# Performance work log

Measured on AMD Instinct MI355X. Metric: run time of the kernel, lower is better.

The kernel has to match this reference:

```python
import jax, jax.numpy as jnp
import numpy as np


def _lstm(x, h0, c0, Wih, Whh, b):
    """Single-layer LSTM, batch_first input x: [B,T,D]. PyTorch gate order i,f,g,o.
    Returns (h_seq [T,B,H], h_T [B,H], c_T [B,H])."""
    xs = jnp.swapaxes(x, 0, 1)  # [T,B,D]

    def step(carry, xt):
        h, c = carry
        gates = xt @ Wih.T + h @ Whh.T + b  # [B,4H]
        i, f, g, o = jnp.split(gates, 4, axis=-1)
        c = jax.nn.sigmoid(f) * c + jax.nn.sigmoid(i) * jnp.tanh(g)
        h = jax.nn.sigmoid(o) * jnp.tanh(c)
        return (h, c), h

    (h, c), hs = jax.lax.scan(step, (h0, c0), xs)
    return hs, h, c


def setup_inputs() -> dict:
    key = jax.random.key(0)
    ks = jax.random.split(key, 16)
    B, T, Tf, Tu = 256, 365, 15, 76
    Dh, Df, Du, H = 64, 32, 16, 256
    s = 1.0 / np.sqrt(H)  # torch-style uniform scale, approximated with scaled normals
    return {
        "x_d": jax.random.normal(ks[0], (B, T, Dh), jnp.float32),
        "x_f": jax.random.normal(ks[1], (B, Tf, Df), jnp.float32),
        "x_ff": jax.random.normal(ks[2], (B, Tu, Du), jnp.float32),
        "enc_Wih": jax.random.normal(ks[3], (4 * H, Dh), jnp.float32) * s,
        "enc_Whh": jax.random.normal(ks[4], (4 * H, H), jnp.float32) * s,
        "enc_b": jax.random.normal(ks[5], (4 * H,), jnp.float32) * s,
        "decf_Wih": jax.random.normal(ks[6], (4 * H, Df), jnp.float32) * s,
        "decf_Whh": jax.random.normal(ks[7], (4 * H, H), jnp.float32) * s,
        "decf_b": jax.random.normal(ks[8], (4 * H,), jnp.float32) * s,
        "decu_Wih": jax.random.normal(ks[9], (4 * H, Du), jnp.float32) * s,
        "decu_Whh": jax.random.normal(ks[10], (4 * H, H), jnp.float32) * s,
        "decu_b": jax.random.normal(ks[11], (4 * H,), jnp.float32) * s,
        "head_W": jax.random.normal(ks[12], (1, H), jnp.float32) * s,
        "head_b": jax.random.normal(ks[13], (1,), jnp.float32) * s,
    }


def reference(x_d, x_f, x_ff, enc_Wih, enc_Whh, enc_b,
              decf_Wih, decf_Whh, decf_b, decu_Wih, decu_Whh, decu_b,
              head_W, head_b):
    B = x_d.shape[0]
    H = enc_Whh.shape[1]
    Tf = x_f.shape[1]
    Tu = x_ff.shape[1]
    horizon = Tf + Tu
    h0 = jnp.zeros((B, H), x_d.dtype)
    c0 = jnp.zeros((B, H), x_d.dtype)

    # Encoder over historical sequence
    _, h, c = _lstm(x_d, h0, c0, enc_Wih, enc_Whh, enc_b)

    # Forecast decoder: one LSTM step per horizon step + linear head (dropout = eval identity)
    hs_f, h, c = _lstm(x_f, h, c, decf_Wih, decf_Whh, decf_b)  # [Tf,B,H]
    out_f = (jnp.einsum('tbh,oh->tbo', hs_f, head_W)[..., 0] + head_b[0]).T  # [B,Tf]

    # Future decoder, continuing the hidden state
    hs_u, h, c = _lstm(x_ff, h, c, decu_Wih, decu_Whh, decu_b)  # [Tu,B,H]
    out_u = (jnp.einsum('tbh,oh->tbo', hs_u, head_W)[..., 0] + head_b[0]).T  # [B,Tu]

    # Faithful to original: both loops write outputs[:, t], so the future loop
    # overwrites the first Tu columns.
    outputs = jnp.zeros((B, horizon), x_d.dtype)
    outputs = outputs.at[:, :Tf].set(out_f)
    outputs = outputs.at[:, :Tu].set(out_u)
    return outputs
```

## Files before the change

### kernel.cpp

```cpp
#include <hip/hip_runtime.h>
#include <stdint.h>


typedef __attribute__((ext_vector_type(8))) short short8;
typedef __attribute__((ext_vector_type(4))) float f32x4;
typedef __attribute__((ext_vector_type(2))) unsigned int u32x2;
typedef __attribute__((ext_vector_type(4))) unsigned int u32x4;

#define L2E 1.4426950408889634f

__device__ __forceinline__ uint16_t f2bf(float f) {
  uint32_t x = __float_as_uint(f);
  x += 0x7fffu + ((x >> 16) & 1u);
  return (uint16_t)(x >> 16);
}
__device__ __forceinline__ uint32_t cvtpk(float lo, float hi) {
  uint32_t r;
  asm("v_cvt_pk_bf16_f32 %0, %1, %2" : "=v"(r) : "v"(lo), "v"(hi));
  return r;
}
__device__ __forceinline__ float bfhalf(uint32_t w, int hi) {
  return __uint_as_float(hi ? (w & 0xffff0000u) : (w << 16));
}
__device__ __forceinline__ f32x4 MFMA(short8 a, short8 b, f32x4 c) {
  return __builtin_amdgcn_mfma_f32_16x16x32_bf16(a, b, c, 0, 0, 0);
}
__device__ __forceinline__ float ex2(float x) { return __builtin_amdgcn_exp2f(x); }
__device__ __forceinline__ float rcp(float x) { return __builtin_amdgcn_rcpf(x); }

__device__ __forceinline__ short8 pack8s(const float* s, float sc) {
  float4 q0 = *(const float4*)s, q1 = *(const float4*)(s + 4);
  u32x4 t;
  t[0] = cvtpk(q0.x * sc, q0.y * sc);
  t[1] = cvtpk(q0.z * sc, q0.w * sc);
  t[2] = cvtpk(q1.x * sc, q1.y * sc);
  t[3] = cvtpk(q1.z * sc, q1.w * sc);
  return *(short8*)&t;
}

__device__ __forceinline__ void lgkm_barrier() {
  __builtin_amdgcn_sched_barrier(0);
  asm volatile("s_waitcnt lgkmcnt(0)" ::: "memory");
  __builtin_amdgcn_s_barrier();
  __builtin_amdgcn_sched_barrier(0);
}
__device__ __forceinline__ void vm_drain4() {
  __builtin_amdgcn_sched_barrier(0);
  asm volatile("s_waitcnt vmcnt(4)" ::: "memory");
  __builtin_amdgcn_sched_barrier(0);
}

__global__ void init_kernel(float* c_state, uint16_t* h_state, float* out) {
  int i = blockIdx.x * 256 + threadIdx.x;
  if (i < 65536) { c_state[i] = 0.f; h_state[i] = 0; }
  if (i < 256 * 91) out[i] = 0.f;
}

template <int DIN>
__device__ __forceinline__ void xproj_body(
    const float* __restrict__ x, const float* __restrict__ Wih,
    const float* __restrict__ bias, uint32_t* __restrict__ xp,
    int T, int blk, int tid) {
  const int w = tid >> 6, l = tid & 63;
  const int l16 = l & 15, lg = l >> 4;
  const int tc = blk >> 1;
  const int sub = blk & 1;
  const int t = tc;
  constexpr int KT = (DIN + 31) / 32;

  short8 bfr[8][KT];
  float4 bias4[8];
#pragma unroll
  for (int ni = 0; ni < 8; ++ni) {
    const int n = (w * 8 + ni) * 16 + l16;
    bias4[ni] = *(const float4*)&bias[(w * 8 + ni) * 16 + lg * 4];
#pragma unroll
    for (int kt = 0; kt < KT; ++kt) {
      const int k0 = kt * 32 + lg * 8;
      short8 fr;
#pragma unroll
      for (int e = 0; e < 8; ++e) fr[e] = 0;
      if (k0 + 8 <= DIN) fr = pack8s(Wih + (size_t)n * DIN + k0, 1.f);
      bfr[ni][kt] = fr;
    }
  }

  for (int mi = 0; mi < 8; ++mi) {
    const int btile = sub * 8 + mi;
    const int b = btile * 16 + l16;
    short8 af[KT];
#pragma unroll
    for (int kt = 0; kt < KT; ++kt) {
      const int k0 = kt * 32 + lg * 8;
      short8 fr;
#pragma unroll
      for (int e = 0; e < 8; ++e) fr[e] = 0;
      if (k0 + 8 <= DIN) fr = pack8s(x + ((size_t)b * T + t) * DIN + k0, 1.f);
      af[kt] = fr;
    }
#pragma unroll
    for (int ni = 0; ni < 8; ++ni) {
      f32x4 acc = {0.f, 0.f, 0.f, 0.f};
#pragma unroll
      for (int kt = 0; kt < KT; ++kt) acc = MFMA(bfr[ni][kt], af[kt], acc);
      const int nt = w * 8 + ni;
      const float sc = ((nt >> 4) == 2) ? (2.f * L2E) : -L2E;
      size_t idx = ((((size_t)tc * 16 + btile) * 64 + nt) * 64 + l) * 2;
      u32x2 v;
      v[0] = cvtpk((acc[0] + bias4[ni].x) * sc, (acc[1] + bias4[ni].y) * sc);
      v[1] = cvtpk((acc[2] + bias4[ni].z) * sc, (acc[3] + bias4[ni].w) * sc);
      *(u32x2*)(xp + idx) = v;
    }
  }
}

template <int DIN>
__global__ __launch_bounds__(512) void xproj_kernel(
    const float* __restrict__ x, const float* __restrict__ Wih,
    const float* __restrict__ bias, uint32_t* __restrict__ xp,
    int t0, int T) {
  const int tid = threadIdx.x;
  const int blk = blockIdx.x + t0 * 2;
  xproj_body<DIN>(x, Wih, bias, xp - (size_t)t0 * 131072, T, blk, tid);
}

__global__ __launch_bounds__(512) void xproj_mega(
    const float* __restrict__ x0, const float* __restrict__ Wih0,
    const float* __restrict__ b0, uint32_t* __restrict__ xp0,
    const float* __restrict__ x1, const float* __restrict__ Wih1,
    const float* __restrict__ b1, uint32_t* __restrict__ xp1,
    const float* __restrict__ x2, const float* __restrict__ Wih2,
    const float* __restrict__ b2, uint32_t* __restrict__ xp2,
    float* __restrict__ out, uint32_t* __restrict__ flags,
    int T0, int T1, int T2) {
  const int tid = threadIdx.x;
  const int n0 = T0 * 2, n1 = T1 * 2, n2 = T2 * 2;
  const int b = blockIdx.x;
  if (b < n0) {
    xproj_body<64>(x0, Wih0, b0, xp0, T0, b, tid);
  } else if (b < n0 + n1) {
    xproj_body<32>(x1, Wih1, b1, xp1, T1, b - n0, tid);
  } else if (b < n0 + n1 + n2) {
    xproj_body<16>(x2, Wih2, b2, xp2, T2, b - n0 - n1, tid);
  } else {
    for (int i = tid; i < 256 * 15; i += 512)
      out[(size_t)(i / 15) * 91 + 76 + (i % 15)] = 0.f;
    if (tid < 96) flags[tid] = 0;
  }
}

template <int DO_HEAD, int ZINIT>
__global__ __launch_bounds__(512, 2) void rec_kernel(
    const uint32_t* __restrict__ xp, const float* __restrict__ Whh,
    float* __restrict__ c_state, uint16_t* __restrict__ h_state,
    float* __restrict__ out, const float* __restrict__ headW,
    const float* __restrict__ headb, int ct, int tcol0) {
  __shared__ short8 B_lds[8 * 16 * 64];
  __shared__ uint16_t h_lds[2][16][264];
  __shared__ float headbuf[2][16][8];

  const int tid = threadIdx.x, w = tid >> 6, l = tid & 63;
  const int l16 = l & 15, lg = l >> 4;
  const int blk = blockIdx.x, b0 = blk * 16;

  short8 bv[48];
#pragma unroll
  for (int g = 0; g < 4; ++g) {
    const float wsc = (g == 2) ? (2.f * L2E) : -L2E;
#pragma unroll
    for (int nt = 0; nt < 2; ++nt)
#pragma unroll
      for (int kt = 0; kt < 8; ++kt) {
        const int row = (g * 16 + w * 2 + nt) * 16 + l16;
        const float* s = Whh + (size_t)row * 256 + kt * 32 + lg * 8;
        short8 fr;
#pragma unroll
        for (int e = 0; e < 8; ++e) fr[e] = (short)f2bf(s[e] * wsc);
        const int tile = g * 2 + nt;
        if (kt <= 5) bv[tile * 6 + kt] = fr;
        else B_lds[(w * 16 + (kt - 6) * 8 + tile) * 64 + l] = fr;
      }
  }

  float c_reg[2][4];
  if (ZINIT) {
#pragma unroll
    for (int nt = 0; nt < 2; ++nt)
#pragma unroll
      for (int j = 0; j < 4; ++j) c_reg[nt][j] = 0.f;
    for (int idx = tid; idx < 16 * 264; idx += 512)
      ((uint16_t*)h_lds)[idx] = 0;
  } else {
#pragma unroll
    for (int nt = 0; nt < 2; ++nt) {
      float4 c4 = *(const float4*)&c_state[(size_t)(b0 + l16) * 256 +
                                           (w * 2 + nt) * 16 + lg * 4];
      c_reg[nt][0] = c4.x; c_reg[nt][1] = c4.y;
      c_reg[nt][2] = c4.z; c_reg[nt][3] = c4.w;
    }
    for (int idx = tid; idx < 16 * 256; idx += 512)
      h_lds[0][idx >> 8][idx & 255] = h_state[(size_t)(b0 + (idx >> 8)) * 256 + (idx & 255)];
  }
  float4 hw4[2];
#pragma unroll
  for (int nt = 0; nt < 2; ++nt)
    hw4[nt] = *(const float4*)&headW[(w * 2 + nt) * 16 + lg * 4];
  const float hb = headb[0];

  const uint32_t* xpb = xp + ((size_t)(blk * 64 + w * 2) * 64 + l) * 2;
  u32x2 xpf[2][4];
#pragma unroll
  for (int nt = 0; nt < 2; ++nt)
#pragma unroll
    for (int g = 0; g < 4; ++g)
      xpf[nt][g] = *(const u32x2*)(xpb + (size_t)g * 2048 + nt * 128);

  __syncthreads();

  for (int t = 0; t < ct; ++t) {
    const int cur = t & 1, nxt = cur ^ 1;
    const int tn = (t + 1 < ct) ? t + 1 : t;
    float hp = 0.f;

#pragma unroll
    for (int nt = 0; nt < 2; ++nt) {
      f32x4 acc[4];
#pragma unroll
      for (int g = 0; g < 4; ++g) {
        f32x4 ai;
        ai[0] = bfhalf(xpf[nt][g][0], 0);
        ai[1] = bfhalf(xpf[nt][g][0], 1);
        ai[2] = bfhalf(xpf[nt][g][1], 0);
        ai[3] = bfhalf(xpf[nt][g][1], 1);
        acc[g] = ai;
      }
#pragma unroll
      for (int kt = 0; kt <= 5; ++kt) {
        short8 hf = *(const short8*)(&h_lds[cur][l16][kt * 32 + lg * 8]);
#pragma unroll
        for (int g = 0; g < 4; ++g)
          acc[g] = MFMA(bv[(g * 2 + nt) * 6 + kt], hf, acc[g]);
      }
#pragma unroll
      for (int kt = 6; kt <= 7; ++kt) {
        short8 hf = *(const short8*)(&h_lds[cur][l16][kt * 32 + lg * 8]);
#pragma unroll
        for (int g = 0; g < 4; ++g)
          acc[g] = MFMA(B_lds[(w * 16 + (kt - 6) * 8 + g * 2 + nt) * 64 + l], hf, acc[g]);
      }

      float hv[4];
#pragma unroll
      for (int j = 0; j < 4; ++j) {
        float ei = ex2(acc[0][j]);
        float ef = ex2(acc[1][j]);
        float eg = ex2(acc[2][j]);
        float eo = ex2(acc[3][j]);
        float eip = 1.f + ei, egp = eg + 1.f, efp = 1.f + ef;
        float d1 = eip * egp;
        float R = rcp(d1 * efp);
        float sitg = (eg - 1.f) * efp * R;
        float cc = fmaf(c_reg[nt][j] * d1, R, sitg);
        c_reg[nt][j] = cc;
        float ec = ex2(cc * (2.f * L2E));
        float hh = (ec - 1.f) * rcp((1.f + eo) * (ec + 1.f));
        hv[j] = hh;
      }
      if (DO_HEAD) {
        hp = fmaf(hv[0], hw4[nt].x, hp); hp = fmaf(hv[1], hw4[nt].y, hp);
        hp = fmaf(hv[2], hw4[nt].z, hp); hp = fmaf(hv[3], hw4[nt].w, hp);
      }
      {
        u32x2 hwrd;
        hwrd[0] = cvtpk(hv[0], hv[1]);
        hwrd[1] = cvtpk(hv[2], hv[3]);
        *(u32x2*)(&h_lds[nxt][l16][(w * 2 + nt) * 16 + lg * 4]) = hwrd;
      }
#pragma unroll
      for (int g = 0; g < 4; ++g)
        xpf[nt][g] = *(const u32x2*)(xpb + (size_t)tn * 131072 + g * 2048 + nt * 128);
    }

    if (DO_HEAD) {
      float s = hp;
      s += __shfl_xor(s, 16);
      s += __shfl_xor(s, 32);
      if (lg == 0) headbuf[t & 1][l16][w] = s;
    }

    lgkm_barrier();

    if (DO_HEAD) {
      if (tid < 16) {
        const float* hbp = headbuf[t & 1][tid];
        float s = hbp[0] + hbp[1] + hbp[2] + hbp[3] + hbp[4] + hbp[5] + hbp[6] + hbp[7];
        out[(size_t)(b0 + tid) * 91 + (tcol0 + t)] = s + hb;
      }
    }
  }

#pragma unroll
  for (int nt = 0; nt < 2; ++nt) {
    float4 c4 = {c_reg[nt][0], c_reg[nt][1], c_reg[nt][2], c_reg[nt][3]};
    *(float4*)&c_state[(size_t)(b0 + l16) * 256 + (w * 2 + nt) * 16 + lg * 4] = c4;
  }
  for (int idx = tid; idx < 16 * 256; idx += 512)
    h_state[(size_t)(b0 + (idx >> 8)) * 256 + (idx & 255)] = h_lds[ct & 1][idx >> 8][idx & 255];
}

template <int DO_HEAD>
__global__ __launch_bounds__(512, 2) void rec_split(
    const uint32_t* __restrict__ xp, const float* __restrict__ Whh,
    float* __restrict__ c_state, uint16_t* __restrict__ h_state,
    float* __restrict__ out, const float* __restrict__ headW,
    const float* __restrict__ headb, uint32_t* __restrict__ flags,
    unsigned long long* __restrict__ hx, uint32_t* __restrict__ hxh,
    int ct, int t0, int phase) {
  __shared__ short8 B_lds[64 * 64];
  __shared__ uint16_t h_lds[2][16][264];
  __shared__ float headbuf[16][8];

  const int tid = threadIdx.x, w = tid >> 6, l = tid & 63;
  const int l16 = l & 15, lg = l >> 4;
  const int blk = blockIdx.x;
  const int pair = blk & 15, s = blk >> 4, sp = 1 - s;
  const int b0 = pair * 16;
  const int ctile = s * 8 + w;
  uint32_t* const pflag = flags + (phase * 16 + pair) * 2 + sp;
  uint32_t* const myflag = flags + (phase * 16 + pair) * 2 + s;

  short8 bv[24];
#pragma unroll
  for (int g = 0; g < 4; ++g) {
    const float wsc = (g == 2) ? (2.f * L2E) : -L2E;
#pragma unroll
    for (int kk = 0; kk < 8; ++kk) {
      const int kt = (kk < 4) ? (4 * s + kk) : (4 * sp + (kk - 4));
      const int row = (g * 16 + ctile) * 16 + l16;
      const float* sw = Whh + (size_t)row * 256 + kt * 32 + lg * 8;
      short8 fr;
#pragma unroll
      for (int e = 0; e < 8; ++e) fr[e] = (short)f2bf(sw[e] * wsc);
      if (kk <= 5) bv[g * 6 + kk] = fr;
      else B_lds[(w * 8 + g * 2 + (kk - 6)) * 64 + l] = fr;
    }
  }

  float c_reg[4];
  {
    float4 c4 = *(const float4*)&c_state[(size_t)(b0 + l16) * 256 +
                                         ctile * 16 + lg * 4];
    c_reg[0] = c4.x; c_reg[1] = c4.y; c_reg[2] = c4.z; c_reg[3] = c4.w;
  }
  for (int idx = tid; idx < 16 * 256; idx += 512)
    h_lds[0][idx >> 8][idx & 255] = h_state[(size_t)(b0 + (idx >> 8)) * 256 + (idx & 255)];
  float4 hw4 = *(const float4*)&headW[ctile * 16 + lg * 4];
  const float hb = headb[0];

  const uint32_t* xpb = xp + ((size_t)(pair * 64 + ctile) * 64 + l) * 2;
  u32x2 xpf[4];
#pragma unroll
  for (int g = 0; g < 4; ++g)
    xpf[g] = *(const u32x2*)(xpb + (size_t)g * 2048);

  __syncthreads();

  u32x2 h_last;
  h_last[0] = 0; h_last[1] = 0;
  float hsum_prev = 0.f;

  for (int t = 0; t < ct; ++t) {
    const int cur = t & 1, nxt = cur ^ 1;
    const int tn = (t + 1 < ct) ? t + 1 : t;
    const int par = t & 1;

    unsigned long long pv = 0ull;
    if (t > 0) {
      const uint32_t tgt = (uint32_t)(t0 + t);
      __builtin_amdgcn_sched_barrier(0);
      uint32_t f;
      do {
        f = __hip_atomic_load(pflag, __ATOMIC_RELAXED, __HIP_MEMORY_SCOPE_AGENT);
      } while ((int)(f - tgt) < 0);
      __builtin_amdgcn_sched_barrier(0);
      pv = __hip_atomic_load(
          hx + ((size_t)((pair * 2 + sp) * 2 + ((t - 1) & 1)) * 512) +
              (w * 4 + lg) * 16 + l16,
          __ATOMIC_RELAXED, __HIP_MEMORY_SCOPE_AGENT);
      if (DO_HEAD && s == 0 && tid < 16) {
        uint32_t pp = __hip_atomic_load(
            hxh + ((pair * 2 + sp) * 2 + ((t - 1) & 1)) * 16 + tid,
            __ATOMIC_RELAXED, __HIP_MEMORY_SCOPE_AGENT);
        out[(size_t)(b0 + tid) * 91 + (t0 + t - 1)] =
            hsum_prev + __uint_as_float(pp) + hb;
      }
    }

    f32x4 acc[4];
#pragma unroll
    for (int g = 0; g < 4; ++g) {
      f32x4 ai;
      ai[0] = bfhalf(xpf[g][0], 0);
      ai[1] = bfhalf(xpf[g][0], 1);
      ai[2] = bfhalf(xpf[g][1], 0);
      ai[3] = bfhalf(xpf[g][1], 1);
      acc[g] = ai;
    }
#pragma unroll
    for (int kk = 0; kk < 4; ++kk) {
      short8 hf = *(const short8*)(&h_lds[cur][l16][(4 * s + kk) * 32 + lg * 8]);
#pragma unroll
      for (int g = 0; g < 4; ++g)
        acc[g] = MFMA(bv[g * 6 + kk], hf, acc[g]);
    }

    if (t > 0) {
      u32x2 pw;
      pw[0] = (uint32_t)pv;
      pw[1] = (uint32_t)(pv >> 32);
      *(u32x2*)(&h_lds[cur][l16][sp * 128 + w * 16 + lg * 4]) = pw;
      lgkm_barrier();
    }

#pragma unroll
    for (int kk = 0; kk < 4; ++kk) {
      short8 hf = *(const short8*)(&h_lds[cur][l16][(4 * sp + kk) * 32 + lg * 8]);
#pragma unroll
      for (int g = 0; g < 4; ++g) {
        if (kk < 2) acc[g] = MFMA(bv[g * 6 + 4 + kk], hf, acc[g]);
        else acc[g] = MFMA(B_lds[(w * 8 + g * 2 + (kk - 2)) * 64 + l], hf, acc[g]);
      }
    }

    float hv[4];
#pragma unroll
    for (int j = 0; j < 4; ++j) {
      float ei = ex2(acc[0][j]);
      float ef = ex2(acc[1][j]);
      float eg = ex2(acc[2][j]);
      float eo = ex2(acc[3][j]);
      float eip = 1.f + ei, egp = eg + 1.f, efp = 1.f + ef;
      float d1 = eip * egp;
      float R = rcp(d1 * efp);
      float sitg = (eg - 1.f) * efp * R;
      float cc = fmaf(c_reg[j] * d1, R, sitg);
      c_reg[j] = cc;
      float ec = ex2(cc * (2.f * L2E));
      float hh = (ec - 1.f) * rcp((1.f + eo) * (ec + 1.f));
      hv[j] = hh;
    }

    h_last[0] = cvtpk(hv[0], hv[1]);
    h_last[1] = cvtpk(hv[2], hv[3]);
    *(u32x2*)(&h_lds[nxt][l16][ctile * 16 + lg * 4]) = h_last;
    {
      unsigned long long v64 =
          ((unsigned long long)h_last[1] << 32) | (unsigned long long)h_last[0];
      __hip_atomic_store(
          hx + ((size_t)((pair * 2 + s) * 2 + par) * 512) + (w * 4 + lg) * 16 + l16,
          v64, __ATOMIC_RELAXED, __HIP_MEMORY_SCOPE_AGENT);
    }

#pragma unroll
    for (int g = 0; g < 4; ++g)
      xpf[g] = *(const u32x2*)(xpb + (size_t)tn * 131072 + g * 2048);

    if (DO_HEAD) {
      float hp = fmaf(hv[0], hw4.x, fmaf(hv[1], hw4.y,
                 fmaf(hv[2], hw4.z, hv[3] * hw4.w)));
      hp += __shfl_xor(hp, 16);
      hp += __shfl_xor(hp, 32);
      if (lg == 0) headbuf[l16][w] = hp;
    }

    vm_drain4();
    lgkm_barrier();

    if (DO_HEAD) {
      if (tid < 16) {
        const float* hbp = headbuf[tid];
        hsum_prev = hbp[0] + hbp[1] + hbp[2] + hbp[3] +
                    hbp[4] + hbp[5] + hbp[6] + hbp[7];
        __hip_atomic_store(hxh + ((pair * 2 + s) * 2 + par) * 16 + tid,
                           __float_as_uint(hsum_prev), __ATOMIC_RELAXED,
                           __HIP_MEMORY_SCOPE_AGENT);
      }
      vm_drain4();
    }
    if (tid == 0)
      __hip_atomic_store(myflag, (uint32_t)(t0 + t + 1), __ATOMIC_RELAXED,
                         __HIP_MEMORY_SCOPE_AGENT);
  }

  {
    float4 c4 = {c_reg[0], c_reg[1], c_reg[2], c_reg[3]};
    *(float4*)&c_state[(size_t)(b0 + l16) * 256 + ctile * 16 + lg * 4] = c4;
  }

  if (s == 0) {
    const uint32_t tgt = (uint32_t)(t0 + ct);
    __builtin_amdgcn_sched_barrier(0);
    uint32_t f;
    do {
      f = __hip_atomic_load(pflag, __ATOMIC_RELAXED, __HIP_MEMORY_SCOPE_AGENT);
    } while ((int)(f - tgt) < 0);
    __builtin_amdgcn_sched_barrier(0);
    unsigned long long pv = __hip_atomic_load(
        hx + ((size_t)((pair * 2 + sp) * 2 + ((ct - 1) & 1)) * 512) +
            (w * 4 + lg) * 16 + l16,
        __ATOMIC_RELAXED, __HIP_MEMORY_SCOPE_AGENT);
    u32x2 pw;
    pw[0] = (uint32_t)pv;
    pw[1] = (uint32_t)(pv >> 32);
    *(u32x2*)&h_state[(size_t)(b0 + l16) * 256 + 128 + w * 16 + lg * 4] = pw;
    *(u32x2*)&h_state[(size_t)(b0 + l16) * 256 + w * 16 + lg * 4] = h_last;
    if (DO_HEAD && tid < 16) {
      uint32_t pp = __hip_atomic_load(
          hxh + ((pair * 2 + sp) * 2 + ((ct - 1) & 1)) * 16 + tid,
          __ATOMIC_RELAXED, __HIP_MEMORY_SCOPE_AGENT);
      out[(size_t)(b0 + tid) * 91 + (t0 + ct - 1)] =
          hsum_prev + __uint_as_float(pp) + hb;
    }
  }
}

extern "C" void kernel_launch(void* const* d_in, const int* in_sizes, int n_in,
                              void* d_out, int out_size, void* d_ws, size_t ws_size,
                              hipStream_t stream) {
  const float* headW = (const float*)d_in[12];
  const float* headb = (const float*)d_in[13];
  float* out = (float*)d_out;
  char* ws = (char*)d_ws;

  const int T0 = in_sizes[0] / (256 * 64);
  const int T1 = in_sizes[1] / (256 * 32);
  const int T2 = in_sizes[2] / (256 * 16);
  const size_t s0 = (size_t)T0 << 19, s1 = (size_t)T1 << 19, s2 = (size_t)T2 << 19;
  const size_t hdr = 667648;

  if (ws_size >= hdr + s0 + s1 + s2) {
    float* c_state = (float*)ws;
    uint16_t* h_state = (uint16_t*)(ws + 262144);
    uint32_t* flags = (uint32_t*)(ws + 393216);
    unsigned long long* hx = (unsigned long long*)(ws + 397312);
    uint32_t* hxh = (uint32_t*)(ws + 659456);
    uint32_t* xp0 = (uint32_t*)(ws + hdr);
    uint32_t* xp1 = (uint32_t*)(ws + hdr + s0);
    uint32_t* xp2 = (uint32_t*)(ws + hdr + s0 + s1);

    const int nblk = T0 * 2 + T1 * 2 + T2 * 2 + 1;
    xproj_mega<<<dim3(nblk), 512, 0, stream>>>(
        (const float*)d_in[0], (const float*)d_in[3], (const float*)d_in[5], xp0,
        (const float*)d_in[1], (const float*)d_in[6], (const float*)d_in[8], xp1,
        (const float*)d_in[2], (const float*)d_in[9], (const float*)d_in[11], xp2,
        out, flags, T0, T1, T2);
    rec_kernel<0, 1><<<16, 512, 0, stream>>>(xp0, (const float*)d_in[4], c_state,
                                             h_state, out, headW, headb, T0, 0);
    rec_split<0><<<32, 512, 0, stream>>>(xp1, (const float*)d_in[7], c_state,
                                         h_state, out, headW, headb, flags, hx,
                                         hxh, T1, 0, 1);
    rec_split<1><<<32, 512, 0, stream>>>(xp2, (const float*)d_in[10], c_state,
                                         h_state, out, headW, headb, flags, hx,
                                         hxh, T2, 0, 2);
    return;
  }

  float* c_state = (float*)ws;
  uint16_t* h_state = (uint16_t*)(ws + 262144);
  uint32_t* xp = (uint32_t*)(ws + 393216);

  int ct_max = 1;
  if (ws_size > 393216 + 512 * 1024) {
    size_t c = (ws_size - 393216) / (512 * 1024);
    ct_max = (c > 365) ? 365 : (int)c;
  }

  init_kernel<<<256, 256, 0, stream>>>(c_state, h_state, out);

  struct Phase { const float* x; const float* Wih; const float* Whh; const float* b; int T; int D; int head; };
  Phase ph[3] = {
      {(const float*)d_in[0], (const float*)d_in[3], (const float*)d_in[4], (const float*)d_in[5], T0, 64, 0},
      {(const float*)d_in[1], (const float*)d_in[6], (const float*)d_in[7], (const float*)d_in[8], T1, 32, 0},
      {(const float*)d_in[2], (const float*)d_in[9], (const float*)d_in[10], (const float*)d_in[11], T2, 16, 1},
  };

  for (int pi = 0; pi < 3; ++pi) {
    const Phase& P = ph[pi];
    for (int t0 = 0; t0 < P.T; t0 += ct_max) {
      int ct = (P.T - t0 < ct_max) ? (P.T - t0) : ct_max;
      dim3 g(ct * 2);
      if (P.D == 64)
        xproj_kernel<64><<<g, 512, 0, stream>>>(P.x, P.Wih, P.b, xp, t0, P.T);
      else if (P.D == 32)
        xproj_kernel<32><<<g, 512, 0, stream>>>(P.x, P.Wih, P.b, xp, t0, P.T);
      else
        xproj_kernel<16><<<g, 512, 0, stream>>>(P.x, P.Wih, P.b, xp, t0, P.T);
      if (P.head)
        rec_kernel<1, 0><<<16, 512, 0, stream>>>(xp, P.Whh, c_state, h_state, out,
                                                 headW, headb, ct, t0);
      else
        rec_kernel<0, 0><<<16, 512, 0, stream>>>(xp, P.Whh, c_state, h_state, out,
                                                 headW, headb, ct, t0);
    }
  }
}
```

Before: 1.206 ms.

## Fuse forecast and future decoder LSTM phases into one persistent split kernel

Merges the two rec_split launches (forecast decoder and future decoder) into a single kernel that loops over both phases. The hidden and cell state stay in registers and LDS between phases instead of being written to global memory and reloaded, and one launch boundary goes away. Each phase now has its own exchange buffers and flag sets, which enlarges the workspace header. In exchange, Whh for the second phase is converted to bf16 inside the kernel between phases, and a small LDS copy aligns the h double-buffer parity.

```diff
diff --git a/kernel.cpp b/kernel.cpp
--- a/kernel.cpp
+++ b/kernel.cpp
@@ -308,14 +308,14 @@
     h_state[(size_t)(b0 + (idx >> 8)) * 256 + (idx & 255)] = h_lds[ct & 1][idx >> 8][idx & 255];
 }
 
-template <int DO_HEAD>
-__global__ __launch_bounds__(512, 2) void rec_split(
-    const uint32_t* __restrict__ xp, const float* __restrict__ Whh,
-    float* __restrict__ c_state, uint16_t* __restrict__ h_state,
+__global__ __launch_bounds__(512, 2) void rec_split2(
+    const uint32_t* __restrict__ xp1g, const uint32_t* __restrict__ xp2g,
+    const float* __restrict__ Whh1, const float* __restrict__ Whh2,
+    const float* __restrict__ c_state, const uint16_t* __restrict__ h_state,
     float* __restrict__ out, const float* __restrict__ headW,
     const float* __restrict__ headb, uint32_t* __restrict__ flags,
     unsigned long long* __restrict__ hx, uint32_t* __restrict__ hxh,
-    int ct, int t0, int phase) {
+    int T1, int T2) {
   __shared__ short8 B_lds[64 * 64];
   __shared__ uint16_t h_lds[2][16][264];
   __shared__ float headbuf[16][8];
@@ -326,25 +326,6 @@
   const int pair = blk & 15, s = blk >> 4, sp = 1 - s;
   const int b0 = pair * 16;
   const int ctile = s * 8 + w;
-  uint32_t* const pflag = flags + (phase * 16 + pair) * 2 + sp;
-  uint32_t* const myflag = flags + (phase * 16 + pair) * 2 + s;
-
-  short8 bv[24];
-#pragma unroll
-  for (int g = 0; g < 4; ++g) {
-    const float wsc = (g == 2) ? (2.f * L2E) : -L2E;
-#pragma unroll
-    for (int kk = 0; kk < 8; ++kk) {
-      const int kt = (kk < 4) ? (4 * s + kk) : (4 * sp + (kk - 4));
-      const int row = (g * 16 + ctile) * 16 + l16;
-      const float* sw = Whh + (size_t)row * 256 + kt * 32 + lg * 8;
-      short8 fr;
-#pragma unroll
-      for (int e = 0; e < 8; ++e) fr[e] = (short)f2bf(sw[e] * wsc);
-      if (kk <= 5) bv[g * 6 + kk] = fr;
-      else B_lds[(w * 8 + g * 2 + (kk - 6)) * 64 + l] = fr;
-    }
-  }
 
   float c_reg[4];
   {
@@ -357,170 +338,209 @@
   float4 hw4 = *(const float4*)&headW[ctile * 16 + lg * 4];
   const float hb = headb[0];
 
-  const uint32_t* xpb = xp + ((size_t)(pair * 64 + ctile) * 64 + l) * 2;
-  u32x2 xpf[4];
-#pragma unroll
-  for (int g = 0; g < 4; ++g)
-    xpf[g] = *(const u32x2*)(xpb + (size_t)g * 2048);
-
-  __syncthreads();
-
-  u32x2 h_last;
-  h_last[0] = 0; h_last[1] = 0;
   float hsum_prev = 0.f;
 
-  for (int t = 0; t < ct; ++t) {
-    const int cur = t & 1, nxt = cur ^ 1;
-    const int tn = (t + 1 < ct) ? t + 1 : t;
-    const int par = t & 1;
-
-    unsigned long long pv = 0ull;
-    if (t > 0) {
-      const uint32_t tgt = (uint32_t)(t0 + t);
+#pragma unroll
+  for (int p = 0; p < 2; ++p) {
+    const float* Whh = p ? Whh2 : Whh1;
+    const uint32_t* xp = p ? xp2g : xp1g;
+    const int ct = p ? T2 : T1;
+    const bool headf = (p == 1);
+    uint32_t* const pflag = flags + ((1 + p) * 16 + pair) * 2 + sp;
+    uint32_t* const myflag = flags + ((1 + p) * 16 + pair) * 2 + s;
+    unsigned long long* const hxp = hx + (size_t)p * 32768;
+    uint32_t* const hxhp = hxh + p * 1024;
+
+    short8 bv[24];
+#pragma unroll
+    for (int g = 0; g < 4; ++g) {
+      const float wsc = (g == 2) ? (2.f * L2E) : -L2E;
+#pragma unroll
+      for (int kk = 0; kk < 8; ++kk) {
+        const int kt = (kk < 4) ? (4 * s + kk) : (4 * sp + (kk - 4));
+        const int row = (g * 16 + ctile) * 16 + l16;
+        const float* sw = Whh + (size_t)row * 256 + kt * 32 + lg * 8;
+        short8 fr;
+#pragma unroll
+        for (int e = 0; e < 8; ++e) fr[e] = (short)f2bf(sw[e] * wsc);
+        if (kk <= 5) bv[g * 6 + kk] = fr;
+        else B_lds[(w * 8 + g * 2 + (kk - 6)) * 64 + l] = fr;
+      }
+    }
+
+    const uint32_t* xpb = xp + ((size_t)(pair * 64 + ctile) * 64 + l) * 2;
+    u32x2 xpf[4];
+#pragma unroll
+    for (int g = 0; g < 4; ++g)
+      xpf[g] = *(const u32x2*)(xpb + (size_t)g * 2048);
+
+    __syncthreads();
+
+    u32x2 h_last; h_last[0] = 0; h_last[1] = 0;
+
+    for (int t = 0; t < ct; ++t) {
+      const int cur = t & 1, nxt = cur ^ 1;
+      const int tn = (t + 1 < ct) ? t + 1 : t;
+      const int par = t & 1;
+
+      unsigned long long pv = 0ull;
+      if (t > 0) {
+        const uint32_t tgt = (uint32_t)t;
+        __builtin_amdgcn_sched_barrier(0);
+        uint32_t f;
+        do {
+          f = __hip_atomic_load(pflag, __ATOMIC_RELAXED, __HIP_MEMORY_SCOPE_AGENT);
+        } while ((int)(f - tgt) < 0);
+        __builtin_amdgcn_sched_barrier(0);
+        pv = __hip_atomic_load(
+            hxp + ((size_t)((pair * 2 + sp) * 2 + ((t - 1) & 1)) * 512) +
+                (w * 4 + lg) * 16 + l16,
+            __ATOMIC_RELAXED, __HIP_MEMORY_SCOPE_AGENT);
+        if (headf && s == 0 && tid < 16) {
+          uint32_t pp = __hip_atomic_load(
+              hxhp + ((pair * 2 + sp) * 2 + ((t - 1) & 1)) * 16 + tid,
+              __ATOMIC_RELAXED, __HIP_MEMORY_SCOPE_AGENT);
+          out[(size_t)(b0 + tid) * 91 + (t - 1)] =
+              hsum_prev + __uint_as_float(pp) + hb;
+        }
+      }
+
+      f32x4 acc[4];
+#pragma unroll
+      for (int g = 0; g < 4; ++g) {
+        f32x4 ai;
+        ai[0] = bfhalf(xpf[g][0], 0);
+        ai[1] = bfhalf(xpf[g][0], 1);
+        ai[2] = bfhalf(xpf[g][1], 0);
+        ai[3] = bfhalf(xpf[g][1], 1);
+        acc[g] = ai;
+      }
+#pragma unroll
+      for (int kk = 0; kk < 4; ++kk) {
+        short8 hf = *(const short8*)(&h_lds[cur][l16][(4 * s + kk) * 32 + lg * 8]);
+#pragma unroll
+        for (int g = 0; g < 4; ++g)
+          acc[g] = MFMA(bv[g * 6 + kk], hf, acc[g]);
+      }
+
+      if (t > 0) {
+        u32x2 pw;
+        pw[0] = (uint32_t)pv;
+        pw[1] = (uint32_t)(pv >> 32);
+        *(u32x2*)(&h_lds[cur][l16][sp * 128 + w * 16 + lg * 4]) = pw;
+        lgkm_barrier();
+      }
+
+#pragma unroll
+      for (int kk = 0; kk < 4; ++kk) {
+        short8 hf = *(const short8*)(&h_lds[cur][l16][(4 * sp + kk) * 32 + lg * 8]);
+#pragma unroll
+        for (int g = 0; g < 4; ++g) {
+          if (kk < 2) acc[g] = MFMA(bv[g * 6 + 4 + kk], hf, acc[g]);
+          else acc[g] = MFMA(B_lds[(w * 8 + g * 2 + (kk - 2)) * 64 + l], hf, acc[g]);
+        }
+      }
+
+      float hv[4];
+#pragma unroll
+      for (int j = 0; j < 4; ++j) {
+        float ei = ex2(acc[0][j]);
+        float ef = ex2(acc[1][j]);
+        float eg = ex2(acc[2][j]);
+        float eo = ex2(acc[3][j]);
+        float eip = 1.f + ei, egp = eg + 1.f, efp = 1.f + ef;
+        float d1 = eip * egp;
+        float R = rcp(d1 * efp);
+        float sitg = (eg - 1.f) * efp * R;
+        float cc = fmaf(c_reg[j] * d1, R, sitg);
+        c_reg[j] = cc;
+        float ec = ex2(cc * (2.f * L2E));
+        float hh = (ec - 1.f) * rcp((1.f + eo) * (ec + 1.f));
+        hv[j] = hh;
+      }
+
+      h_last[0] = cvtpk(hv[0], hv[1]);
+      h_last[1] = cvtpk(hv[2], hv[3]);
+      *(u32x2*)(&h_lds[nxt][l16][ctile * 16 + lg * 4]) = h_last;
+      {
+        unsigned long long v64 =
+            ((unsigned long long)h_last[1] << 32) | (unsigned long long)h_last[0];
+        __hip_atomic_store(
+            hxp + ((size_t)((pair * 2 + s) * 2 + par) * 512) + (w * 4 + lg) * 16 + l16,
+            v64, __ATOMIC_RELAXED, __HIP_MEMORY_SCOPE_AGENT);
+      }
+
+#pragma unroll
+      for (int g = 0; g < 4; ++g)
+        xpf[g] = *(const u32x2*)(xpb + (size_t)tn * 131072 + g * 2048);
+
+      if (headf) {
+        float hp = fmaf(hv[0], hw4.x, fmaf(hv[1], hw4.y,
+                   fmaf(hv[2], hw4.z, hv[3] * hw4.w)));
+        hp += __shfl_xor(hp, 16);
+        hp += __shfl_xor(hp, 32);
+        if (lg == 0) headbuf[l16][w] = hp;
+      }
+
+      vm_drain4();
+      lgkm_barrier();
+
+      if (headf) {
+        if (tid < 16) {
+          const float* hbp = headbuf[tid];
+          hsum_prev = hbp[0] + hbp[1] + hbp[2] + hbp[3] +
+                      hbp[4] + hbp[5] + hbp[6] + hbp[7];
+          __hip_atomic_store(hxhp + ((pair * 2 + s) * 2 + par) * 16 + tid,
+                             __float_as_uint(hsum_prev), __ATOMIC_RELAXED,
+                             __HIP_MEMORY_SCOPE_AGENT);
+        }
+        vm_drain4();
+      }
+      if (tid == 0)
+        __hip_atomic_store(myflag, (uint32_t)(t + 1), __ATOMIC_RELAXED,
+                           __HIP_MEMORY_SCOPE_AGENT);
+    }
+
+    if (p == 0) {
+      const uint32_t tgt = (uint32_t)ct;
       __builtin_amdgcn_sched_barrier(0);
       uint32_t f;
       do {
         f = __hip_atomic_load(pflag, __ATOMIC_RELAXED, __HIP_MEMORY_SCOPE_AGENT);
       } while ((int)(f - tgt) < 0);
       __builtin_amdgcn_sched_barrier(0);
-      pv = __hip_atomic_load(
-          hx + ((size_t)((pair * 2 + sp) * 2 + ((t - 1) & 1)) * 512) +
+      unsigned long long pv = __hip_atomic_load(
+          hxp + ((size_t)((pair * 2 + sp) * 2 + ((ct - 1) & 1)) * 512) +
               (w * 4 + lg) * 16 + l16,
           __ATOMIC_RELAXED, __HIP_MEMORY_SCOPE_AGENT);
-      if (DO_HEAD && s == 0 && tid < 16) {
-        uint32_t pp = __hip_atomic_load(
-            hxh + ((pair * 2 + sp) * 2 + ((t - 1) & 1)) * 16 + tid,
-            __ATOMIC_RELAXED, __HIP_MEMORY_SCOPE_AGENT);
-        out[(size_t)(b0 + tid) * 91 + (t0 + t - 1)] =
-            hsum_prev + __uint_as_float(pp) + hb;
-      }
-    }
-
-    f32x4 acc[4];
-#pragma unroll
-    for (int g = 0; g < 4; ++g) {
-      f32x4 ai;
-      ai[0] = bfhalf(xpf[g][0], 0);
-      ai[1] = bfhalf(xpf[g][0], 1);
-      ai[2] = bfhalf(xpf[g][1], 0);
-      ai[3] = bfhalf(xpf[g][1], 1);
-      acc[g] = ai;
-    }
-#pragma unroll
-    for (int kk = 0; kk < 4; ++kk) {
-      short8 hf = *(const short8*)(&h_lds[cur][l16][(4 * s + kk) * 32 + lg * 8]);
-#pragma unroll
-      for (int g = 0; g < 4; ++g)
-        acc[g] = MFMA(bv[g * 6 + kk], hf, acc[g]);
-    }
-
-    if (t > 0) {
+      const int fb = ct & 1;
       u32x2 pw;
       pw[0] = (uint32_t)pv;
       pw[1] = (uint32_t)(pv >> 32);
-      *(u32x2*)(&h_lds[cur][l16][sp * 128 + w * 16 + lg * 4]) = pw;
+      *(u32x2*)(&h_lds[fb][l16][sp * 128 + w * 16 + lg * 4]) = pw;
       lgkm_barrier();
-    }
-
-#pragma unroll
-    for (int kk = 0; kk < 4; ++kk) {
-      short8 hf = *(const short8*)(&h_lds[cur][l16][(4 * sp + kk) * 32 + lg * 8]);
-#pragma unroll
-      for (int g = 0; g < 4; ++g) {
-        if (kk < 2) acc[g] = MFMA(bv[g * 6 + 4 + kk], hf, acc[g]);
-        else acc[g] = MFMA(B_lds[(w * 8 + g * 2 + (kk - 2)) * 64 + l], hf, acc[g]);
-      }
-    }
-
-    float hv[4];
-#pragma unroll
-    for (int j = 0; j < 4; ++j) {
-      float ei = ex2(acc[0][j]);
-      float ef = ex2(acc[1][j]);
-      float eg = ex2(acc[2][j]);
-      float eo = ex2(acc[3][j]);
-      float eip = 1.f + ei, egp = eg + 1.f, efp = 1.f + ef;
-      float d1 = eip * egp;
-      float R = rcp(d1 * efp);
-      float sitg = (eg - 1.f) * efp * R;
-      float cc = fmaf(c_reg[j] * d1, R, sitg);
-      c_reg[j] = cc;
-      float ec = ex2(cc * (2.f * L2E));
-      float hh = (ec - 1.f) * rcp((1.f + eo) * (ec + 1.f));
-      hv[j] = hh;
-    }
-
-    h_last[0] = cvtpk(hv[0], hv[1]);
-    h_last[1] = cvtpk(hv[2], hv[3]);
-    *(u32x2*)(&h_lds[nxt][l16][ctile * 16 + lg * 4]) = h_last;
-    {
-      unsigned long long v64 =
-          ((unsigned long long)h_last[1] << 32) | (unsigned long long)h_last[0];
-      __hip_atomic_store(
-          hx + ((size_t)((pair * 2 + s) * 2 + par) * 512) + (w * 4 + lg) * 16 + l16,
-          v64, __ATOMIC_RELAXED, __HIP_MEMORY_SCOPE_AGENT);
-    }
-
-#pragma unroll
-    for (int g = 0; g < 4; ++g)
-      xpf[g] = *(const u32x2*)(xpb + (size_t)tn * 131072 + g * 2048);
-
-    if (DO_HEAD) {
-      float hp = fmaf(hv[0], hw4.x, fmaf(hv[1], hw4.y,
-                 fmaf(hv[2], hw4.z, hv[3] * hw4.w)));
-      hp += __shfl_xor(hp, 16);
-      hp += __shfl_xor(hp, 32);
-      if (lg == 0) headbuf[l16][w] = hp;
-    }
-
-    vm_drain4();
-    lgkm_barrier();
-
-    if (DO_HEAD) {
-      if (tid < 16) {
-        const float* hbp = headbuf[tid];
-        hsum_prev = hbp[0] + hbp[1] + hbp[2] + hbp[3] +
-                    hbp[4] + hbp[5] + hbp[6] + hbp[7];
-        __hip_atomic_store(hxh + ((pair * 2 + s) * 2 + par) * 16 + tid,
-                           __float_as_uint(hsum_prev), __ATOMIC_RELAXED,
-                           __HIP_MEMORY_SCOPE_AGENT);
-      }
-      vm_drain4();
-    }
-    if (tid == 0)
-      __hip_atomic_store(myflag, (uint32_t)(t0 + t + 1), __ATOMIC_RELAXED,
-                         __HIP_MEMORY_SCOPE_AGENT);
-  }
-
-  {
-    float4 c4 = {c_reg[0], c_reg[1], c_reg[2], c_reg[3]};
-    *(float4*)&c_state[(size_t)(b0 + l16) * 256 + ctile * 16 + lg * 4] = c4;
-  }
-
-  if (s == 0) {
-    const uint32_t tgt = (uint32_t)(t0 + ct);
-    __builtin_amdgcn_sched_barrier(0);
+      if (fb != 0) {
+        for (int idx = tid; idx < 1024; idx += 512) {
+          const int r = idx >> 6, c4v = (idx & 63) * 4;
+          *(u32x2*)(&h_lds[0][r][c4v]) = *(const u32x2*)(&h_lds[1][r][c4v]);
+        }
+      }
+      lgkm_barrier();
+    }
+  }
+
+  if (s == 0 && tid < 16) {
+    uint32_t* const pflag2 = flags + (2 * 16 + pair) * 2 + sp;
+    const uint32_t tgt = (uint32_t)T2;
     uint32_t f;
     do {
-      f = __hip_atomic_load(pflag, __ATOMIC_RELAXED, __HIP_MEMORY_SCOPE_AGENT);
+      f = __hip_atomic_load(pflag2, __ATOMIC_RELAXED, __HIP_MEMORY_SCOPE_AGENT);
     } while ((int)(f - tgt) < 0);
-    __builtin_amdgcn_sched_barrier(0);
-    unsigned long long pv = __hip_atomic_load(
-        hx + ((size_t)((pair * 2 + sp) * 2 + ((ct - 1) & 1)) * 512) +
-            (w * 4 + lg) * 16 + l16,
+    uint32_t pp = __hip_atomic_load(
+        hxh + 1024 + ((pair * 2 + sp) * 2 + ((T2 - 1) & 1)) * 16 + tid,
         __ATOMIC_RELAXED, __HIP_MEMORY_SCOPE_AGENT);
-    u32x2 pw;
-    pw[0] = (uint32_t)pv;
-    pw[1] = (uint32_t)(pv >> 32);
-    *(u32x2*)&h_state[(size_t)(b0 + l16) * 256 + 128 + w * 16 + lg * 4] = pw;
-    *(u32x2*)&h_state[(size_t)(b0 + l16) * 256 + w * 16 + lg * 4] = h_last;
-    if (DO_HEAD && tid < 16) {
-      uint32_t pp = __hip_atomic_load(
-          hxh + ((pair * 2 + sp) * 2 + ((ct - 1) & 1)) * 16 + tid,
-          __ATOMIC_RELAXED, __HIP_MEMORY_SCOPE_AGENT);
-      out[(size_t)(b0 + tid) * 91 + (t0 + ct - 1)] =
-          hsum_prev + __uint_as_float(pp) + hb;
-    }
+    out[(size_t)(b0 + tid) * 91 + (T2 - 1)] =
+        hsum_prev + __uint_as_float(pp) + hb;
   }
 }
 
@@ -536,14 +556,14 @@
   const int T1 = in_sizes[1] / (256 * 32);
   const int T2 = in_sizes[2] / (256 * 16);
   const size_t s0 = (size_t)T0 << 19, s1 = (size_t)T1 << 19, s2 = (size_t)T2 << 19;
-  const size_t hdr = 667648;
+  const size_t hdr = 929792;
 
   if (ws_size >= hdr + s0 + s1 + s2) {
     float* c_state = (float*)ws;
     uint16_t* h_state = (uint16_t*)(ws + 262144);
     uint32_t* flags = (uint32_t*)(ws + 393216);
     unsigned long long* hx = (unsigned long long*)(ws + 397312);
-    uint32_t* hxh = (uint32_t*)(ws + 659456);
+    uint32_t* hxh = (uint32_t*)(ws + 921600);
     uint32_t* xp0 = (uint32_t*)(ws + hdr);
     uint32_t* xp1 = (uint32_t*)(ws + hdr + s0);
     uint32_t* xp2 = (uint32_t*)(ws + hdr + s0 + s1);
@@ -556,12 +576,9 @@
         out, flags, T0, T1, T2);
     rec_kernel<0, 1><<<16, 512, 0, stream>>>(xp0, (const float*)d_in[4], c_state,
                                              h_state, out, headW, headb, T0, 0);
-    rec_split<0><<<32, 512, 0, stream>>>(xp1, (const float*)d_in[7], c_state,
-                                         h_state, out, headW, headb, flags, hx,
-                                         hxh, T1, 0, 1);
-    rec_split<1><<<32, 512, 0, stream>>>(xp2, (const float*)d_in[10], c_state,
-                                         h_state, out, headW, headb, flags, hx,
-                                         hxh, T2, 0, 2);
+    rec_split2<<<32, 512, 0, stream>>>(xp1, xp2, (const float*)d_in[7],
+                                       (const float*)d_in[10], c_state, h_state,
+                                       out, headW, headb, flags, hx, hxh, T1, T2);
     return;
   }
 
```

After: 1.196 ms (median of 2 runs). No clear change (-0.8%).
